# Performance work log

Measured on AMD Instinct MI355X. Metric: run time of the kernel, lower is better.

## Reference

```python
import jax, jax.numpy as jnp
import numpy as np

B, N, INIT_DIM, DIMS, K, RADIUS = 8, 4096, 6, 64, 32, 0.1
EPS = 1e-5


def layer_norm(x, g, b):
    m = jnp.mean(x, axis=-1, keepdims=True)
    v = jnp.mean((x - m) ** 2, axis=-1, keepdims=True)
    return (x - m) * jax.lax.rsqrt(v + EPS) * g + b


def query_ball(sqrdists, radius, k):
    # sqrdists: [B, S, N] squared distances. PointNet++ ball query:
    # indices outside the ball -> N, sort, take first k, backfill with first idx.
    n = sqrdists.shape[-1]
    idx = jnp.arange(n, dtype=jnp.int32)
    gi = jnp.where(sqrdists <= radius * radius, idx[None, None, :], n)
    gi = jnp.sort(gi, axis=-1)[..., :k]
    first = gi[..., :1]
    return jnp.where(gi == n, first, gi)  # [B, S, k]


def setup_inputs() -> dict:
    key = jax.random.key(0)
    ks = jax.random.split(key, 10)
    inputs = jax.random.normal(ks[0], (B, N, INIT_DIM), dtype=jnp.float32)
    coordinates = jax.random.uniform(ks[1], (B, N, 3), dtype=jnp.float32)
    # squared pairwise distances via |a|^2 + |b|^2 - 2 a.b (avoids [B,N,N,3] temp)
    sq = jnp.sum(coordinates ** 2, axis=-1)
    distance_matrices = (sq[:, :, None] + sq[:, None, :]
                         - 2.0 * jnp.einsum('bnc,bmc->bnm', coordinates, coordinates))
    distance_matrices = jnp.maximum(distance_matrices, 0.0)
    s1 = 1.0 / np.sqrt(INIT_DIM)
    s2 = 1.0 / np.sqrt(2 * DIMS)
    W1 = jax.random.uniform(ks[2], (INIT_DIM, DIMS), minval=-s1, maxval=s1)
    b1 = jax.random.uniform(ks[3], (DIMS,), minval=-s1, maxval=s1)
    g1 = jnp.ones((DIMS,), jnp.float32)
    be1 = jnp.zeros((DIMS,), jnp.float32)
    W2 = jax.random.uniform(ks[4], (2 * DIMS, DIMS), minval=-s2, maxval=s2)
    b2 = jax.random.uniform(ks[5], (DIMS,), minval=-s2, maxval=s2)
    g2 = jnp.ones((DIMS,), jnp.float32)
    be2 = jnp.zeros((DIMS,), jnp.float32)
    return {"inputs": inputs, "coordinates": coordinates,
            "distance_matrices": distance_matrices,
            "W1": W1, "b1": b1, "g1": g1, "be1": be1,
            "W2": W2, "b2": b2, "g2": g2, "be2": be2}


def reference(inputs, coordinates, distance_matrices, W1, b1, g1, be1, W2, b2, g2, be2):
    # embedding: Linear -> LayerNorm -> ReLU
    x = jax.nn.relu(layer_norm(inputs @ W1 + b1, g1, be1))  # [B,N,D]
    idx = query_ball(distance_matrices, RADIUS, K)           # [B,N,K] int32
    ball = jax.vmap(lambda xb, ib: xb[ib])(x, idx)           # [B,N,K,D]
    xc = x[:, :, None, :]                                    # [B,N,1,D]
    rel = ball - xc
    comb = jnp.concatenate([rel, jnp.broadcast_to(xc, rel.shape)], axis=-1)  # [B,N,K,2D]
    y = jax.nn.relu(layer_norm(comb @ W2 + b2, g2, be2))     # [B,N,K,D]
    return jnp.max(y, axis=-2)                               # [B,N,D]
```

## Files before the change

### kernel.cpp

```cpp
#include <hip/hip_runtime.h>
#include <cstdint>
#include <cstddef>

#define BB 8
#define NN 4096
#define IDIM 6
#define DIMS 64
#define KNB 32
#define BN (BB * NN)

static constexpr float LN_EPS = 1e-5f;

template<int CTRL>
__device__ __forceinline__ float dpp_xadd(float v) {
    int r = __builtin_amdgcn_update_dpp(0, __float_as_int(v), CTRL, 0xF, 0xF, true);
    return v + __int_as_float(r);
}
template<int OFFS>
__device__ __forceinline__ float swz_xadd(float v) {
    int r = __builtin_amdgcn_ds_swizzle(__float_as_int(v), OFFS);
    return v + __int_as_float(r);
}
__device__ __forceinline__ float wsum64(float v) {
    v = dpp_xadd<0xB1>(v);
    v = dpp_xadd<0x4E>(v);
    v = swz_xadd<0x101F>(v);
    v = dpp_xadd<0x128>(v);
    v = swz_xadd<0x401F>(v);
    v += __shfl_xor(v, 32, 64);
    return v;
}

__global__ __launch_bounds__(256, 4) void k1_feat(
    const float* __restrict__ inp, const float* __restrict__ coords,
    const float* __restrict__ W1, const float* __restrict__ b1,
    const float* __restrict__ g1, const float* __restrict__ be1,
    const float* __restrict__ W2, const float* __restrict__ b2,
    float* __restrict__ a_buf, float* __restrict__ c_buf,
    float* __restrict__ Sa_buf, float4* __restrict__ cq_buf)
{
    const int lane = threadIdx.x & 63;
    const int p = (blockIdx.x << 2) + (threadIdx.x >> 6);

    if (threadIdx.x < 4) {
        const int pp = (blockIdx.x << 2) + threadIdx.x;
        const float x = coords[3 * pp], y = coords[3 * pp + 1], z = coords[3 * pp + 2];
        cq_buf[pp] = make_float4(x, y, z, fmaf(z, z, fmaf(y, y, x * x)));
    }

    const float* ip = inp + (size_t)p * IDIM;
    float h = b1[lane];
#pragma unroll
    for (int j = 0; j < IDIM; ++j)
        h = fmaf(ip[j], W1[j * DIMS + lane], h);
    const float mean = wsum64(h) * (1.0f / DIMS);
    const float dv = h - mean;
    const float var = wsum64(dv * dv) * (1.0f / DIMS);
    const float x = fmaxf(dv * rsqrtf(var + LN_EPS) * g1[lane] + be1[lane], 0.0f);

    float a = 0.0f, cp = 0.0f;
    const int xi = __float_as_int(x);
#pragma unroll 8
    for (int j = 0; j < DIMS; ++j) {
        const int sj = __builtin_amdgcn_readlane(xi, j);
        if (sj != 0) {
            const float xj = __int_as_float(sj);
            a  = fmaf(xj, W2[j * DIMS + lane], a);
            cp = fmaf(xj, W2[(DIMS + j) * DIMS + lane], cp);
        }
    }
    const float c = cp + b2[lane] - a;
    a_buf[(size_t)p * DIMS + lane] = a;
    c_buf[(size_t)p * DIMS + lane] = c;
    const float sa = wsum64(a);
    if (lane == 0) Sa_buf[p] = sa;
}

__global__ __launch_bounds__(512, 4) void k23(
    const float4* __restrict__ cq, const float* __restrict__ DM,
    const float* __restrict__ a_buf, const float* __restrict__ c_buf,
    const float* __restrict__ Sa_buf, const float* __restrict__ g2,
    const float* __restrict__ be2, float* __restrict__ outp)
{
    __shared__ float4 sc[NN];

    const int bid = ((blockIdx.x & 7) << 9) + (blockIdx.x >> 3);
    const int lane = threadIdx.x & 63;
    const int w = threadIdx.x >> 6;
    const int row = (bid << 3) + w;
    const int b = row >> 12;
    const int n = row & (NN - 1);

    const float4* cb = cq + ((size_t)b << 12);
    for (int i = threadIdx.x; i < NN; i += 512)
        sc[i] = cb[i];
    __syncthreads();

    const float4 pn = sc[n];
    const float R2 = (float)(0.1 * 0.1);
    const float thr = R2 - pn.w;
    const float BAND = 1e-4f;
    const float* __restrict__ dmrow = DM + (size_t)row * NN;

    int cnt = 0, first = n, myidx = 0;
    for (int mb = 0; mb < NN; mb += 64) {
        const int mm = mb + lane;
        const float4 pm = sc[mm];
        const float dot = fmaf(pn.z, pm.z, fmaf(pn.y, pm.y, pn.x * pm.x));
        const float e = fmaf(-2.0f, dot, pm.w);
        bool within = (e <= thr);
        const bool band = fabsf(e - thr) <= BAND;
        if (__any(band)) {
            if (band) within = (dmrow[mm] <= R2);
        }
        unsigned long long msk = __ballot(within);
        if (msk) {
            if (cnt == 0) first = mb + (int)__builtin_ctzll(msk);
            while (msk && cnt < KNB) {
                const int t = (int)__builtin_ctzll(msk);
                if (lane == cnt) myidx = mb + t;
                msk &= msk - 1;
                ++cnt;
            }
            if (cnt >= KNB) break;
        }
    }
    if (lane >= cnt && lane < KNB) myidx = first;

    const float cv = c_buf[(size_t)row * DIMS + lane];
    const float Sc = wsum64(cv);
    const float gg = g2[lane], bb = be2[lane];
    const float* __restrict__ abase = a_buf + (((size_t)b << 12) * DIMS);
    const float* __restrict__ Sab = Sa_buf + (b << 12);
    const int mix = myidx;

    float om0 = 0.0f, om1 = 0.0f, om2 = 0.0f, om3 = 0.0f;
#pragma unroll 2
    for (int k = 0; k < KNB; k += 4) {
        const int m0 = __builtin_amdgcn_readlane(mix, k + 0);
        const int m1 = __builtin_amdgcn_readlane(mix, k + 1);
        const int m2 = __builtin_amdgcn_readlane(mix, k + 2);
        const int m3 = __builtin_amdgcn_readlane(mix, k + 3);
        const float mu0 = (Sab[m0] + Sc) * (1.0f / DIMS);
        const float mu1 = (Sab[m1] + Sc) * (1.0f / DIMS);
        const float mu2 = (Sab[m2] + Sc) * (1.0f / DIMS);
        const float mu3 = (Sab[m3] + Sc) * (1.0f / DIMS);
        const float d0 = abase[(size_t)m0 * DIMS + lane] + cv - mu0;
        const float d1 = abase[(size_t)m1 * DIMS + lane] + cv - mu1;
        const float d2 = abase[(size_t)m2 * DIMS + lane] + cv - mu2;
        const float d3 = abase[(size_t)m3 * DIMS + lane] + cv - mu3;
        const float q0 = wsum64(d0 * d0);
        const float q1 = wsum64(d1 * d1);
        const float q2 = wsum64(d2 * d2);
        const float q3 = wsum64(d3 * d3);
        const float y0 = d0 * rsqrtf(q0 * (1.0f / DIMS) + LN_EPS) * gg + bb;
        const float y1 = d1 * rsqrtf(q1 * (1.0f / DIMS) + LN_EPS) * gg + bb;
        const float y2 = d2 * rsqrtf(q2 * (1.0f / DIMS) + LN_EPS) * gg + bb;
        const float y3 = d3 * rsqrtf(q3 * (1.0f / DIMS) + LN_EPS) * gg + bb;
        om0 = fmaxf(om0, y0);
        om1 = fmaxf(om1, y1);
        om2 = fmaxf(om2, y2);
        om3 = fmaxf(om3, y3);
    }
    outp[(size_t)row * DIMS + lane] =
        fmaxf(fmaxf(fmaxf(om0, om1), fmaxf(om2, om3)), 0.0f);
}

extern "C" void kernel_launch(void* const* d_in, const int* in_sizes, int n_in,
                              void* d_out, int out_size, void* d_ws, size_t ws_size,
                              hipStream_t stream)
{
    const float* inp    = (const float*)d_in[0];
    const float* coords = (const float*)d_in[1];
    const float* DM     = (const float*)d_in[2];
    const float* W1     = (const float*)d_in[3];
    const float* b1v    = (const float*)d_in[4];
    const float* g1     = (const float*)d_in[5];
    const float* be1    = (const float*)d_in[6];
    const float* W2     = (const float*)d_in[7];
    const float* b2v    = (const float*)d_in[8];
    const float* g2     = (const float*)d_in[9];
    const float* be2    = (const float*)d_in[10];
    float* out = (float*)d_out;

    char* ws = (char*)d_ws;
    float*  a_buf  = (float*)(ws);
    float*  c_buf  = (float*)(ws + (size_t)BN * DIMS * 4);
    float*  Sa_buf = (float*)(ws + (size_t)2 * BN * DIMS * 4);
    float4* cq     = (float4*)(ws + (size_t)2 * BN * DIMS * 4
                                  + (size_t)BN * 4);

    k1_feat<<<dim3(BN / 4), dim3(256), 0, stream>>>(
        inp, coords, W1, b1v, g1, be1, W2, b2v, a_buf, c_buf, Sa_buf, cq);
    k23<<<dim3(BN / 8), dim3(512), 0, stream>>>(
        cq, DM, a_buf, c_buf, Sa_buf, g2, be2, out);
}
```

Baseline: 770.5 us.

## Replace brute-force ball query with uniform grid cell lookup

Builds a 10x10x10 uniform grid per batch with count, scan and scatter kernels, then has each query scan only the 27 neighbouring cells. Hits are sorted with a wave-wide bitonic sort to recover the first-K-by-index order, and a full linear scan runs only when more than 64 hits are found. This removes the per-row sweep over all 4096 points and the shared-memory staging of every coordinate. In exchange it adds four extra launches, global atomics and a sort, and it depends on coordinates lying in [0,1).

```diff
diff --git a/kernel.cpp b/kernel.cpp
--- a/kernel.cpp
+++ b/kernel.cpp
@@ -8,8 +8,10 @@
 #define DIMS 64
 #define KNB 32
 #define BN (BB * NN)
+#define NCELL 1024
 
 static constexpr float LN_EPS = 1e-5f;
+static constexpr float INV_SIDE = 1.0f / 0.11f;
 
 template<int CTRL>
 __device__ __forceinline__ float dpp_xadd(float v) {
@@ -31,23 +33,87 @@
     return v;
 }
 
+template<int K, int J>
+__device__ __forceinline__ void bstep(int& v, int lane) {
+    const int o = __shfl_xor(v, J, 64);
+    const bool up = (lane & K) == 0;
+    const bool lower = (lane & J) == 0;
+    v = (lower == up) ? min(v, o) : max(v, o);
+}
+__device__ __forceinline__ void sort64(int& v, int lane) {
+    bstep<2,1>(v,lane);
+    bstep<4,2>(v,lane);  bstep<4,1>(v,lane);
+    bstep<8,4>(v,lane);  bstep<8,2>(v,lane);  bstep<8,1>(v,lane);
+    bstep<16,8>(v,lane); bstep<16,4>(v,lane); bstep<16,2>(v,lane); bstep<16,1>(v,lane);
+    bstep<32,16>(v,lane); bstep<32,8>(v,lane); bstep<32,4>(v,lane); bstep<32,2>(v,lane); bstep<32,1>(v,lane);
+    bstep<64,32>(v,lane); bstep<64,16>(v,lane); bstep<64,8>(v,lane); bstep<64,4>(v,lane); bstep<64,2>(v,lane); bstep<64,1>(v,lane);
+}
+
+__device__ __forceinline__ int cell_of(float x, float y, float z) {
+    const int cx = min((int)(x * INV_SIDE), 9);
+    const int cy = min((int)(y * INV_SIDE), 9);
+    const int cz = min((int)(z * INV_SIDE), 9);
+    return cx * 100 + cy * 10 + cz;
+}
+
+__global__ __launch_bounds__(256) void k_count(const float* __restrict__ coords,
+                                               int* __restrict__ counts,
+                                               float4* __restrict__ cq)
+{
+    const int p = blockIdx.x * 256 + threadIdx.x;
+    const float x = coords[3 * p], y = coords[3 * p + 1], z = coords[3 * p + 2];
+    cq[p] = make_float4(x, y, z, fmaf(z, z, fmaf(y, y, x * x)));
+    const int b = p >> 12;
+    atomicAdd(&counts[(b << 10) + cell_of(x, y, z)], 1);
+}
+
+__global__ __launch_bounds__(256) void k_scan(const int* __restrict__ counts,
+                                              int* __restrict__ starts,
+                                              int* __restrict__ cursor)
+{
+    __shared__ int ssum[256];
+    const int b = blockIdx.x, t = threadIdx.x;
+    const int base = (b << 10) + (t << 2);
+    const int c0 = counts[base], c1 = counts[base + 1];
+    const int c2 = counts[base + 2], c3 = counts[base + 3];
+    const int s = c0 + c1 + c2 + c3;
+    ssum[t] = s;
+    __syncthreads();
+    int acc = s;
+    for (int off = 1; off < 256; off <<= 1) {
+        const int v = (t >= off) ? ssum[t - off] : 0;
+        __syncthreads();
+        acc += v; ssum[t] = acc;
+        __syncthreads();
+    }
+    int run = acc - s;
+    starts[base] = run; cursor[base] = run; run += c0;
+    starts[base + 1] = run; cursor[base + 1] = run; run += c1;
+    starts[base + 2] = run; cursor[base + 2] = run; run += c2;
+    starts[base + 3] = run; cursor[base + 3] = run;
+}
+
+__global__ __launch_bounds__(256) void k_scatter(const float* __restrict__ coords,
+                                                 int* __restrict__ cursor,
+                                                 int* __restrict__ csr)
+{
+    const int p = blockIdx.x * 256 + threadIdx.x;
+    const float x = coords[3 * p], y = coords[3 * p + 1], z = coords[3 * p + 2];
+    const int b = p >> 12;
+    const int pos = atomicAdd(&cursor[(b << 10) + cell_of(x, y, z)], 1);
+    csr[(b << 12) + pos] = p & (NN - 1);
+}
+
 __global__ __launch_bounds__(256, 4) void k1_feat(
-    const float* __restrict__ inp, const float* __restrict__ coords,
-    const float* __restrict__ W1, const float* __restrict__ b1,
-    const float* __restrict__ g1, const float* __restrict__ be1,
-    const float* __restrict__ W2, const float* __restrict__ b2,
+    const float* __restrict__ inp, const float* __restrict__ W1,
+    const float* __restrict__ b1, const float* __restrict__ g1,
+    const float* __restrict__ be1, const float* __restrict__ W2,
+    const float* __restrict__ b2,
     float* __restrict__ a_buf, float* __restrict__ c_buf,
-    float* __restrict__ Sa_buf, float4* __restrict__ cq_buf)
+    float* __restrict__ Sa_buf)
 {
     const int lane = threadIdx.x & 63;
     const int p = (blockIdx.x << 2) + (threadIdx.x >> 6);
-
-    if (threadIdx.x < 4) {
-        const int pp = (blockIdx.x << 2) + threadIdx.x;
-        const float x = coords[3 * pp], y = coords[3 * pp + 1], z = coords[3 * pp + 2];
-        cq_buf[pp] = make_float4(x, y, z, fmaf(z, z, fmaf(y, y, x * x)));
-    }
-
     const float* ip = inp + (size_t)p * IDIM;
     float h = b1[lane];
 #pragma unroll
@@ -79,10 +145,14 @@
 __global__ __launch_bounds__(512, 4) void k23(
     const float4* __restrict__ cq, const float* __restrict__ DM,
     const float* __restrict__ a_buf, const float* __restrict__ c_buf,
-    const float* __restrict__ Sa_buf, const float* __restrict__ g2,
-    const float* __restrict__ be2, float* __restrict__ outp)
-{
-    __shared__ float4 sc[NN];
+    const float* __restrict__ Sa_buf, const int* __restrict__ starts,
+    const int* __restrict__ counts, const int* __restrict__ csr,
+    const float* __restrict__ g2, const float* __restrict__ be2,
+    float* __restrict__ outp)
+{
+    __shared__ int p_tab[8][32];
+    __shared__ int s_tab[8][32];
+    __shared__ int hits[8][64];
 
     const int bid = ((blockIdx.x & 7) << 9) + (blockIdx.x >> 3);
     const int lane = threadIdx.x & 63;
@@ -91,56 +161,107 @@
     const int b = row >> 12;
     const int n = row & (NN - 1);
 
-    const float4* cb = cq + ((size_t)b << 12);
-    for (int i = threadIdx.x; i < NN; i += 512)
-        sc[i] = cb[i];
-    __syncthreads();
-
-    const float4 pn = sc[n];
+    const float4* __restrict__ cqb = cq + ((size_t)b << 12);
+    const float4 pn = cqb[n];
     const float R2 = (float)(0.1 * 0.1);
     const float thr = R2 - pn.w;
     const float BAND = 1e-4f;
     const float* __restrict__ dmrow = DM + (size_t)row * NN;
 
-    int cnt = 0, first = n, myidx = 0;
-    for (int mb = 0; mb < NN; mb += 64) {
-        const int mm = mb + lane;
-        const float4 pm = sc[mm];
-        const float dot = fmaf(pn.z, pm.z, fmaf(pn.y, pm.y, pn.x * pm.x));
-        const float e = fmaf(-2.0f, dot, pm.w);
-        bool within = (e <= thr);
-        const bool band = fabsf(e - thr) <= BAND;
-        if (__any(band)) {
-            if (band) within = (dmrow[mm] <= R2);
-        }
-        unsigned long long msk = __ballot(within);
-        if (msk) {
-            if (cnt == 0) first = mb + (int)__builtin_ctzll(msk);
-            while (msk && cnt < KNB) {
-                const int t = (int)__builtin_ctzll(msk);
-                if (lane == cnt) myidx = mb + t;
-                msk &= msk - 1;
+    const int cx = min((int)(pn.x * INV_SIDE), 9);
+    const int cy = min((int)(pn.y * INV_SIDE), 9);
+    const int cz = min((int)(pn.z * INV_SIDE), 9);
+
+    int cnt_i = 0, start_i = 0;
+    if (lane < 27) {
+        const int dx = lane / 9 - 1, dy = (lane / 3) % 3 - 1, dz = lane % 3 - 1;
+        const int X = cx + dx, Y = cy + dy, Z = cz + dz;
+        if ((unsigned)X <= 9u && (unsigned)Y <= 9u && (unsigned)Z <= 9u) {
+            const int cid = (b << 10) + X * 100 + Y * 10 + Z;
+            cnt_i = counts[cid];
+            start_i = starts[cid];
+        }
+    }
+    int incl = cnt_i;
+#pragma unroll
+    for (int s = 1; s < 64; s <<= 1) {
+        const int tv = __shfl_up(incl, s, 64);
+        if (lane >= s) incl += tv;
+    }
+    const int T = __builtin_amdgcn_readlane(incl, 63);
+    if (lane < 32) {
+        p_tab[w][lane] = (lane < 27) ? (incl - cnt_i) : T;
+        s_tab[w][lane] = start_i;
+    }
+    __syncthreads();
+
+    int cnt = 0;
+    for (int tb = 0; tb < T; tb += 64) {
+        const int t = tb + lane;
+        int mm = 0;
+        bool within = false;
+        if (t < T) {
+            int c = 0;
+#pragma unroll
+            for (int s = 16; s >= 1; s >>= 1)
+                if (p_tab[w][c + s] <= t) c += s;
+            const int j = t - p_tab[w][c];
+            mm = csr[(b << 12) + s_tab[w][c] + j];
+            const float4 pm = cqb[mm];
+            const float dot = fmaf(pn.z, pm.z, fmaf(pn.y, pm.y, pn.x * pm.x));
+            const float e = fmaf(-2.0f, dot, pm.w);
+            within = (e <= thr);
+            if (fabsf(e - thr) <= BAND) within = (dmrow[mm] <= R2);
+        }
+        const unsigned long long msk = __ballot(within);
+        if (within) {
+            const int pos = cnt + __popcll(msk & ((1ull << lane) - 1ull));
+            if (pos < 64) hits[w][pos] = mm;
+        }
+        cnt += __popcll(msk);
+    }
+    __syncthreads();
+
+    int myidx = 0x7fffffff;
+    if (cnt <= 64) {
+        if (lane < cnt) myidx = hits[w][lane];
+    } else {
+        cnt = 0;
+        for (int mb = 0; mb < NN && cnt < KNB; mb += 64) {
+            const int mmf = mb + lane;
+            const float4 pm = cqb[mmf];
+            const float dot = fmaf(pn.z, pm.z, fmaf(pn.y, pm.y, pn.x * pm.x));
+            const float e = fmaf(-2.0f, dot, pm.w);
+            bool wi = (e <= thr);
+            if (fabsf(e - thr) <= BAND) wi = (dmrow[mmf] <= R2);
+            unsigned long long m2 = __ballot(wi);
+            while (m2 && cnt < KNB) {
+                const int src = (int)__builtin_ctzll(m2);
+                if (lane == cnt) myidx = mb + src;
+                m2 &= m2 - 1;
                 ++cnt;
             }
-            if (cnt >= KNB) break;
-        }
-    }
-    if (lane >= cnt && lane < KNB) myidx = first;
+        }
+    }
+    sort64(myidx, lane);
+    const int KK = min(cnt, KNB);
 
     const float cv = c_buf[(size_t)row * DIMS + lane];
     const float Sc = wsum64(cv);
     const float gg = g2[lane], bb = be2[lane];
-    const float* __restrict__ abase = a_buf + (((size_t)b << 12) * DIMS);
+    const float* __restrict__ abase = a_buf + ((size_t)(b << 12) * DIMS);
     const float* __restrict__ Sab = Sa_buf + (b << 12);
     const int mix = myidx;
 
     float om0 = 0.0f, om1 = 0.0f, om2 = 0.0f, om3 = 0.0f;
-#pragma unroll 2
-    for (int k = 0; k < KNB; k += 4) {
-        const int m0 = __builtin_amdgcn_readlane(mix, k + 0);
-        const int m1 = __builtin_amdgcn_readlane(mix, k + 1);
-        const int m2 = __builtin_amdgcn_readlane(mix, k + 2);
-        const int m3 = __builtin_amdgcn_readlane(mix, k + 3);
+    for (int k = 0; k < KK; k += 4) {
+        const int ka = min(k + 1, KK - 1);
+        const int kb2 = min(k + 2, KK - 1);
+        const int kc = min(k + 3, KK - 1);
+        const int m0 = __builtin_amdgcn_readlane(mix, k);
+        const int m1 = __builtin_amdgcn_readlane(mix, ka);
+        const int m2 = __builtin_amdgcn_readlane(mix, kb2);
+        const int m3 = __builtin_amdgcn_readlane(mix, kc);
         const float mu0 = (Sab[m0] + Sc) * (1.0f / DIMS);
         const float mu1 = (Sab[m1] + Sc) * (1.0f / DIMS);
         const float mu2 = (Sab[m2] + Sc) * (1.0f / DIMS);
@@ -184,14 +305,22 @@
     float* out = (float*)d_out;
 
     char* ws = (char*)d_ws;
-    float*  a_buf  = (float*)(ws);
-    float*  c_buf  = (float*)(ws + (size_t)BN * DIMS * 4);
-    float*  Sa_buf = (float*)(ws + (size_t)2 * BN * DIMS * 4);
-    float4* cq     = (float4*)(ws + (size_t)2 * BN * DIMS * 4
-                                  + (size_t)BN * 4);
-
+    size_t off = 0;
+    float*  a_buf  = (float*)(ws + off); off += (size_t)BN * DIMS * 4;
+    float*  c_buf  = (float*)(ws + off); off += (size_t)BN * DIMS * 4;
+    float*  Sa_buf = (float*)(ws + off); off += (size_t)BN * 4;
+    float4* cq     = (float4*)(ws + off); off += (size_t)BN * 16;
+    int*    counts = (int*)(ws + off); off += (size_t)BB * NCELL * 4;
+    int*    starts = (int*)(ws + off); off += (size_t)BB * NCELL * 4;
+    int*    cursor = (int*)(ws + off); off += (size_t)BB * NCELL * 4;
+    int*    csr    = (int*)(ws + off); off += (size_t)BN * 4;
+
+    hipMemsetAsync(counts, 0, (size_t)BB * NCELL * 4, stream);
+    k_count<<<dim3(BN / 256), dim3(256), 0, stream>>>(coords, counts, cq);
+    k_scan<<<dim3(BB), dim3(256), 0, stream>>>(counts, starts, cursor);
+    k_scatter<<<dim3(BN / 256), dim3(256), 0, stream>>>(coords, cursor, csr);
     k1_feat<<<dim3(BN / 4), dim3(256), 0, stream>>>(
-        inp, coords, W1, b1v, g1, be1, W2, b2v, a_buf, c_buf, Sa_buf, cq);
+        inp, W1, b1v, g1, be1, W2, b2v, a_buf, c_buf, Sa_buf);
     k23<<<dim3(BN / 8), dim3(512), 0, stream>>>(
-        cq, DM, a_buf, c_buf, Sa_buf, g2, be2, out);
-}
+        cq, DM, a_buf, c_buf, Sa_buf, starts, counts, csr, g2, be2, out);
+}
```

Result: faster. 685.8 us (-11.0%).
